# Performance work log

Measured on AMD Instinct MI355X. Metric: run time of the kernel, lower is better.

## Reference

```python
import jax, jax.numpy as jnp
from jax import lax
import numpy as np

N_STEPS = 5  # hard-coded truncated history length in the module


def setup_inputs() -> dict:
    key = jax.random.key(0)
    kH, kv, k1, k2, k3 = jax.random.split(key, 5)
    B, S, D = 32, 512, 512
    scale = 1.0 / np.sqrt(D)  # keep tanh/softmax out of saturation
    return {
        "H": jax.random.normal(kH, (B, S, D), dtype=jnp.float32),
        "v": jax.random.normal(kv, (D, 1), dtype=jnp.float32) * scale,
        "W1": jax.random.normal(k1, (D, D), dtype=jnp.float32) * scale,
        "W2": jax.random.normal(k2, (D, D), dtype=jnp.float32) * scale,
        "W3": jax.random.normal(k3, (D, D), dtype=jnp.float32) * scale,
    }


def reference(H, v, W1, W2, W3):
    # H: [B, S, D] -> output [B, S, D] (torch returns list of S tensors [B,1,D])
    B, S, D = H.shape

    def step(carry, ht):  # ht: [B, D]
        H_prev, H_prev_tilde = carry  # each [B, N_STEPS, D]
        # temp: [B, N_STEPS, D]; ht @ W2 broadcasts over the history axis
        temp = jnp.tanh(H_prev @ W1 + (ht @ W2)[:, None, :] + H_prev_tilde @ W3)
        w_t = jax.nn.softmax(temp @ v, axis=1)            # [B, N_STEPS, 1]
        ht_hat = jnp.sum(H_prev_tilde * w_t, axis=1)      # [B, D]
        ht_tilde = ht + jax.nn.relu(ht_hat)               # [B, D]
        H_prev = jnp.concatenate([H_prev[:, 1:, :], ht[:, None, :]], axis=1)
        H_prev_tilde = jnp.concatenate([H_prev_tilde[:, 1:, :], ht_tilde[:, None, :]], axis=1)
        return (H_prev, H_prev_tilde), ht_tilde

    init = (jnp.zeros((B, N_STEPS, D), H.dtype), jnp.zeros((B, N_STEPS, D), H.dtype))
    _, ys = lax.scan(step, init, jnp.swapaxes(H, 0, 1))  # ys: [S, B, D]
    return jnp.swapaxes(ys, 0, 1)  # [B, S, D]
```

## Files before the change

kernel.cpp:

```cpp
#include <hip/hip_runtime.h>


#define BB 32
#define SS 512
#define DD 512
#define NS 5

#define A_ELEMS    ((size_t)BB * SS * DD)
#define EXCH_U64_PER_B 128
#define EXCH_OFF   (A_ELEMS * 4)
#define EXCH_BYTES ((size_t)BB * EXCH_U64_PER_B * 8)
#define WS_NEED    (EXCH_OFF + EXCH_BYTES)

typedef __attribute__((ext_vector_type(4))) float f32x4;

template <int CTRL, int RMASK, int BMASK, bool BC>
__device__ __forceinline__ float dpp_term(float x) {
  return __uint_as_float((unsigned)__builtin_amdgcn_update_dpp(
      0, (int)__float_as_uint(x), CTRL, RMASK, BMASK, BC));
}
__device__ __forceinline__ float wave_sum64(float x) {
  x += dpp_term<0xB1, 0xF, 0xF, true>(x);
  x += dpp_term<0x4E, 0xF, 0xF, true>(x);
  x += dpp_term<0x141, 0xF, 0xF, true>(x);
  x += dpp_term<0x140, 0xF, 0xF, true>(x);
  x += dpp_term<0x142, 0xA, 0xF, false>(x);
  x += dpp_term<0x143, 0xC, 0xF, false>(x);
  return x;
}
__device__ __forceinline__ float group8_sum(float x) {
  x += dpp_term<0xB1, 0xF, 0xF, true>(x);
  x += dpp_term<0x4E, 0xF, 0xF, true>(x);
  x += dpp_term<0x141, 0xF, 0xF, true>(x);
  return x;
}

__global__ void __launch_bounds__(256) th_phase1(
    const float* __restrict__ H, const float* __restrict__ W1,
    const float* __restrict__ W2, float* __restrict__ A, float* __restrict__ B2) {
  const int tid = threadIdx.x;
  const int mt = blockIdx.x >> 3;
  const int nt = blockIdx.x & 7;
  const int m0 = mt << 6, n0 = nt << 6;
  __shared__ float Ht[64][20];
  __shared__ float Wt1[16][64];
  __shared__ float Wt2[16][64];
  const int tx = tid & 15, ty = tid >> 4;
  const int sr = tid >> 2, sk = (tid & 3) << 2;
  const int wr = tid >> 4, wn = (tid & 15) << 2;
  float a1[4][4] = {{0.f}}, a2[4][4] = {{0.f}};

  for (int k0 = 0; k0 < DD; k0 += 16) {
    float4 hv  = *(const float4*)&H[(size_t)(m0 + sr) * DD + k0 + sk];
    float4 w1v = *(const float4*)&W1[(size_t)(k0 + wr) * DD + n0 + wn];
    float4 w2v = *(const float4*)&W2[(size_t)(k0 + wr) * DD + n0 + wn];
    *(float4*)&Ht[sr][sk]  = hv;
    *(float4*)&Wt1[wr][wn] = w1v;
    *(float4*)&Wt2[wr][wn] = w2v;
    __syncthreads();
#pragma unroll
    for (int kq = 0; kq < 16; kq += 4) {
      float hs[4][4];
#pragma unroll
      for (int i = 0; i < 4; ++i) {
        float4 h4 = *(const float4*)&Ht[ty * 4 + i][kq];
        hs[i][0] = h4.x; hs[i][1] = h4.y; hs[i][2] = h4.z; hs[i][3] = h4.w;
      }
#pragma unroll
      for (int kk = 0; kk < 4; ++kk) {
        float4 w1f = *(const float4*)&Wt1[kq + kk][tx * 4];
        float4 w2f = *(const float4*)&Wt2[kq + kk][tx * 4];
#pragma unroll
        for (int i = 0; i < 4; ++i) {
          float h = hs[i][kk];
          a1[i][0] = fmaf(h, w1f.x, a1[i][0]);
          a1[i][1] = fmaf(h, w1f.y, a1[i][1]);
          a1[i][2] = fmaf(h, w1f.z, a1[i][2]);
          a1[i][3] = fmaf(h, w1f.w, a1[i][3]);
          a2[i][0] = fmaf(h, w2f.x, a2[i][0]);
          a2[i][1] = fmaf(h, w2f.y, a2[i][1]);
          a2[i][2] = fmaf(h, w2f.z, a2[i][2]);
          a2[i][3] = fmaf(h, w2f.w, a2[i][3]);
        }
      }
    }
    __syncthreads();
  }
#pragma unroll
  for (int i = 0; i < 4; ++i) {
    float4 o1 = make_float4(a1[i][0], a1[i][1], a1[i][2], a1[i][3]);
    float4 o2 = make_float4(a2[i][0], a2[i][1], a2[i][2], a2[i][3]);
    size_t off = (size_t)(m0 + ty * 4 + i) * DD + n0 + tx * 4;
    *(float4*)&A[off]  = o1;
    *(float4*)&B2[off] = o2;
  }
}

__global__ void __launch_bounds__(512) th_phase2(
    const float* __restrict__ H, const float* __restrict__ v,
    const float* __restrict__ W3, const float* __restrict__ A,
    float* __restrict__ Ob,
    unsigned long long* __restrict__ exch) {
  const int tid = threadIdx.x;
  const int b = blockIdx.x & 31;
  const int g = blockIdx.x >> 5;
  const int q = tid >> 6;
  const int ln = tid & 63;
  const int col = (g << 6) + ln;

  __shared__ float tlds[DD];
  __shared__ float pm[DD];
  __shared__ float wl[8];

  float wa[64];
#pragma unroll
  for (int i = 0; i < 64; ++i)
    wa[i] = W3[(size_t)(q * 64 + i) * DD + col];

  const float* Hb = H + (size_t)b * SS * DD;
  const float* Ab = A + (size_t)b * SS * DD;
  float* Op = Ob + (size_t)b * SS * DD;
  unsigned long long* eb = exch + (size_t)b * EXCH_U64_PER_B;

  float v_col = (q < NS) ? v[col] : 0.f;
  float aA[NS] = {0.f, 0.f, 0.f, 0.f, 0.f};
  float cC[NS] = {0.f, 0.f, 0.f, 0.f, 0.f};
  float tl[NS] = {0.f, 0.f, 0.f, 0.f, 0.f};
  float s4_prev = 0.f;
  float h_cur = Hb[tid];
  float btB = (q < NS) ? Op[DD + col] : 0.f;

  if (tid < NS) wl[tid] = 0.2f;

#pragma unroll 1
  for (int t5 = 0; t5 < 515; t5 += 5) {
#pragma unroll
    for (int p = 0; p < NS; ++p) {
      const int t = t5 + p;
      if (t < SS) {
        const bool pub = (t + 1 < SS);

        float aN_v = 0.f, bt2 = 0.f;
        if (q < NS) {
          aN_v = Ab[(size_t)t * DD + col];
          if (t + 2 < SS) bt2 = Op[(size_t)(t + 2) * DD + col];
        }
        float h_nxt = 0.f;
        if (pub) h_nxt = Hb[(size_t)(t + 1) * DD + tid];

        if (q >= 1 && q < NS && pub) {
          float aa = aA[(p + 1) % NS];
          aa = (q == 2) ? aA[(p + 2) % NS] : aa;
          aa = (q == 3) ? aA[(p + 3) % NS] : aa;
          aa = (q == 4) ? aA[(p + 4) % NS] : aa;
          float cc = cC[(p + 1) % NS];
          cc = (q == 2) ? cC[(p + 2) % NS] : cc;
          cc = (q == 3) ? cC[(p + 3) % NS] : cc;
          cc = (q == 4) ? cC[(p + 4) % NS] : cc;
          float x = aa + btB + cc;
          float e = __expf(2.0f * x);
          float s = (1.0f - 2.0f / (e + 1.0f)) * v_col;
          s = wave_sum64(s);
          if (ln == 63)
            __hip_atomic_store(&eb[(size_t)((t + 1) & 1) * 64 + (q - 1) * 8 + g],
                (unsigned long long)__float_as_uint(s) |
                    ((unsigned long long)(t + 2) << 32),
                __ATOMIC_RELAXED, __HIP_MEMORY_SCOPE_AGENT);
        }

        if (q == 0 && t >= 1) {
          const unsigned long long* wsl = eb + (size_t)(t & 1) * 64;
          float pv = 0.f;
          if (ln < 40) {
            if (!((ln >> 3) == 4 && (ln & 7) == g)) {
              unsigned long long w;
              do {
                w = __hip_atomic_load(&wsl[ln], __ATOMIC_RELAXED,
                                      __HIP_MEMORY_SCOPE_AGENT);
              } while ((unsigned)(w >> 32) != (unsigned)(t + 1));
              pv = __uint_as_float((unsigned)w);
            } else {
              pv = s4_prev;
            }
          }
          pv = group8_sum(pv);
          float sc0 = __shfl(pv, 0, 64);
          float sc1 = __shfl(pv, 8, 64);
          float sc2 = __shfl(pv, 16, 64);
          float sc3 = __shfl(pv, 24, 64);
          float sc4 = __shfl(pv, 32, 64);
          float mx = fmaxf(fmaxf(fmaxf(sc0, sc1), fmaxf(sc2, sc3)), sc4);
          float e0 = __expf(sc0 - mx), e1 = __expf(sc1 - mx);
          float e2 = __expf(sc2 - mx), e3 = __expf(sc3 - mx);
          float e4 = __expf(sc4 - mx);
          float inv = 1.0f / (e0 + e1 + e2 + e3 + e4);
          float wv = e0 * inv;
          wv = (ln == 1) ? e1 * inv : wv;
          wv = (ln == 2) ? e2 * inv : wv;
          wv = (ln == 3) ? e3 * inv : wv;
          wv = (ln == 4) ? e4 * inv : wv;
          if (ln < NS) wl[ln] = wv;
        }
        __syncthreads();

        float w0 = wl[0], w1 = wl[1], w2 = wl[2], w3_ = wl[3], w4 = wl[4];
        float hh = w0 * tl[p];
        hh = fmaf(w1, tl[(p + 1) % NS], hh);
        hh = fmaf(w2, tl[(p + 2) % NS], hh);
        hh = fmaf(w3_, tl[(p + 3) % NS], hh);
        hh = fmaf(w4, tl[(p + 4) % NS], hh);
        float tld = h_cur + fmaxf(hh, 0.f);
        tl[p] = tld;
        tlds[tid] = tld;
        if (g == 0) Op[(size_t)t * DD + tid] = tld;
        asm volatile("s_waitcnt lgkmcnt(0)" ::: "memory");

        float a0 = 0.f, a1 = 0.f, a2 = 0.f, a3 = 0.f;
        const f32x4* tv = (const f32x4*)&tlds[q << 6];
#pragma unroll
        for (int i = 0; i < 16; ++i) {
          f32x4 t4 = tv[i];
          a0 = fmaf(t4.x, wa[4 * i + 0], a0);
          a1 = fmaf(t4.y, wa[4 * i + 1], a1);
          a2 = fmaf(t4.z, wa[4 * i + 2], a2);
          a3 = fmaf(t4.w, wa[4 * i + 3], a3);
        }
        pm[tid] = (a0 + a1) + (a2 + a3);
        __syncthreads();

        if (q < NS) {
          float c = 0.f;
#pragma unroll
          for (int s = 0; s < 8; ++s) c += pm[s * 64 + ln];
          aA[p] = aN_v;
          cC[p] = c;
          if (q == 0 && pub) {
            float x = aN_v + btB + c;
            float e = __expf(2.0f * x);
            float s4 = (1.0f - 2.0f / (e + 1.0f)) * v_col;
            s4 = wave_sum64(s4);
            if (ln == 63)
              __hip_atomic_store(&eb[(size_t)((t + 1) & 1) * 64 + 32 + g],
                  (unsigned long long)__float_as_uint(s4) |
                      ((unsigned long long)(t + 2) << 32),
                  __ATOMIC_RELAXED, __HIP_MEMORY_SCOPE_AGENT);
            s4_prev = __shfl(s4, 63, 64);
          }
          btB = bt2;
        }
        h_cur = h_nxt;
      }
    }
  }
}

extern "C" void kernel_launch(void* const* d_in, const int* in_sizes, int n_in,
                              void* d_out, int out_size, void* d_ws, size_t ws_size,
                              hipStream_t stream) {
  const float* H  = (const float*)d_in[0];
  const float* v  = (const float*)d_in[1];
  const float* W1 = (const float*)d_in[2];
  const float* W2 = (const float*)d_in[3];
  const float* W3 = (const float*)d_in[4];
  float* out = (float*)d_out;

  if (ws_size < WS_NEED) return;

  float* A = (float*)d_ws;
  unsigned long long* exch = (unsigned long long*)((char*)d_ws + EXCH_OFF);

  (void)hipMemsetAsync(exch, 0, EXCH_BYTES, stream);
  hipLaunchKernelGGL(th_phase1, dim3(256 * 8), dim3(256), 0, stream,
                     H, W1, W2, A, out);
  hipLaunchKernelGGL(th_phase2, dim3(BB * 8), dim3(512), 0, stream,
                     H, v, W3, A, out, exch);
}
```

Before: 1.121 ms.

## Fuse H@W1 and H@W2 projections into the recurrent scan kernel

Removes the separate GEMM pre-pass that computed H@W1 and H@W2 into workspace and output memory. The scan kernel now keeps W1 and W2 column slices in registers alongside W3 and computes the per-step projections inside its loop, using extra shared buffers and a one-step lookahead for the W2 term. This drops a large global write and read of intermediates and one kernel launch. In exchange the sequential critical path per step gains two more 512-wide dot products, and register pressure roughly triples (192 weight floats per thread), which risks spilling.

```diff
diff --git a/kernel.cpp b/kernel.cpp
--- a/kernel.cpp
+++ b/kernel.cpp
@@ -6,11 +6,9 @@
 #define DD 512
 #define NS 5
 
-#define A_ELEMS    ((size_t)BB * SS * DD)
 #define EXCH_U64_PER_B 128
-#define EXCH_OFF   (A_ELEMS * 4)
 #define EXCH_BYTES ((size_t)BB * EXCH_U64_PER_B * 8)
-#define WS_NEED    (EXCH_OFF + EXCH_BYTES)
+#define WS_NEED    EXCH_BYTES
 
 typedef __attribute__((ext_vector_type(4))) float f32x4;
 
@@ -35,70 +33,10 @@
   return x;
 }
 
-__global__ void __launch_bounds__(256) th_phase1(
-    const float* __restrict__ H, const float* __restrict__ W1,
-    const float* __restrict__ W2, float* __restrict__ A, float* __restrict__ B2) {
-  const int tid = threadIdx.x;
-  const int mt = blockIdx.x >> 3;
-  const int nt = blockIdx.x & 7;
-  const int m0 = mt << 6, n0 = nt << 6;
-  __shared__ float Ht[64][20];
-  __shared__ float Wt1[16][64];
-  __shared__ float Wt2[16][64];
-  const int tx = tid & 15, ty = tid >> 4;
-  const int sr = tid >> 2, sk = (tid & 3) << 2;
-  const int wr = tid >> 4, wn = (tid & 15) << 2;
-  float a1[4][4] = {{0.f}}, a2[4][4] = {{0.f}};
-
-  for (int k0 = 0; k0 < DD; k0 += 16) {
-    float4 hv  = *(const float4*)&H[(size_t)(m0 + sr) * DD + k0 + sk];
-    float4 w1v = *(const float4*)&W1[(size_t)(k0 + wr) * DD + n0 + wn];
-    float4 w2v = *(const float4*)&W2[(size_t)(k0 + wr) * DD + n0 + wn];
-    *(float4*)&Ht[sr][sk]  = hv;
-    *(float4*)&Wt1[wr][wn] = w1v;
-    *(float4*)&Wt2[wr][wn] = w2v;
-    __syncthreads();
-#pragma unroll
-    for (int kq = 0; kq < 16; kq += 4) {
-      float hs[4][4];
-#pragma unroll
-      for (int i = 0; i < 4; ++i) {
-        float4 h4 = *(const float4*)&Ht[ty * 4 + i][kq];
-        hs[i][0] = h4.x; hs[i][1] = h4.y; hs[i][2] = h4.z; hs[i][3] = h4.w;
-      }
-#pragma unroll
-      for (int kk = 0; kk < 4; ++kk) {
-        float4 w1f = *(const float4*)&Wt1[kq + kk][tx * 4];
-        float4 w2f = *(const float4*)&Wt2[kq + kk][tx * 4];
-#pragma unroll
-        for (int i = 0; i < 4; ++i) {
-          float h = hs[i][kk];
-          a1[i][0] = fmaf(h, w1f.x, a1[i][0]);
-          a1[i][1] = fmaf(h, w1f.y, a1[i][1]);
-          a1[i][2] = fmaf(h, w1f.z, a1[i][2]);
-          a1[i][3] = fmaf(h, w1f.w, a1[i][3]);
-          a2[i][0] = fmaf(h, w2f.x, a2[i][0]);
-          a2[i][1] = fmaf(h, w2f.y, a2[i][1]);
-          a2[i][2] = fmaf(h, w2f.z, a2[i][2]);
-          a2[i][3] = fmaf(h, w2f.w, a2[i][3]);
-        }
-      }
-    }
-    __syncthreads();
-  }
-#pragma unroll
-  for (int i = 0; i < 4; ++i) {
-    float4 o1 = make_float4(a1[i][0], a1[i][1], a1[i][2], a1[i][3]);
-    float4 o2 = make_float4(a2[i][0], a2[i][1], a2[i][2], a2[i][3]);
-    size_t off = (size_t)(m0 + ty * 4 + i) * DD + n0 + tx * 4;
-    *(float4*)&A[off]  = o1;
-    *(float4*)&B2[off] = o2;
-  }
-}
-
-__global__ void __launch_bounds__(512) th_phase2(
+__global__ void __launch_bounds__(512) th_fused(
     const float* __restrict__ H, const float* __restrict__ v,
-    const float* __restrict__ W3, const float* __restrict__ A,
+    const float* __restrict__ W1, const float* __restrict__ W2,
+    const float* __restrict__ W3,
     float* __restrict__ Ob,
     unsigned long long* __restrict__ exch) {
   const int tid = threadIdx.x;
@@ -109,16 +47,23 @@
   const int col = (g << 6) + ln;
 
   __shared__ float tlds[DD];
-  __shared__ float pm[DD];
+  __shared__ float hA[DD];
+  __shared__ float hB[DD];
+  __shared__ float pm0[DD];
+  __shared__ float pm1[DD];
+  __shared__ float pm2[DD];
   __shared__ float wl[8];
 
-  float wa[64];
-#pragma unroll
-  for (int i = 0; i < 64; ++i)
-    wa[i] = W3[(size_t)(q * 64 + i) * DD + col];
+  float wa3[64], wa1[64], wa2[64];
+#pragma unroll
+  for (int i = 0; i < 64; ++i) {
+    const size_t off = (size_t)(q * 64 + i) * DD + col;
+    wa3[i] = W3[off];
+    wa1[i] = W1[off];
+    wa2[i] = W2[off];
+  }
 
   const float* Hb = H + (size_t)b * SS * DD;
-  const float* Ab = A + (size_t)b * SS * DD;
   float* Op = Ob + (size_t)b * SS * DD;
   unsigned long long* eb = exch + (size_t)b * EXCH_U64_PER_B;
 
@@ -128,9 +73,34 @@
   float tl[NS] = {0.f, 0.f, 0.f, 0.f, 0.f};
   float s4_prev = 0.f;
   float h_cur = Hb[tid];
-  float btB = (q < NS) ? Op[DD + col] : 0.f;
+  float h_n1  = Hb[DD + tid];
+  float btB = 0.f;
 
   if (tid < NS) wl[tid] = 0.2f;
+
+  {
+    hB[tid] = h_n1;
+    asm volatile("s_waitcnt lgkmcnt(0)" ::: "memory");
+    float a0 = 0.f, a1 = 0.f, a2 = 0.f, a3 = 0.f;
+    const f32x4* tv = (const f32x4*)&hB[q << 6];
+#pragma unroll
+    for (int i = 0; i < 16; ++i) {
+      f32x4 t4 = tv[i];
+      a0 = fmaf(t4.x, wa2[4 * i + 0], a0);
+      a1 = fmaf(t4.y, wa2[4 * i + 1], a1);
+      a2 = fmaf(t4.z, wa2[4 * i + 2], a2);
+      a3 = fmaf(t4.w, wa2[4 * i + 3], a3);
+    }
+    pm2[tid] = (a0 + a1) + (a2 + a3);
+    __syncthreads();
+    if (q < NS) {
+      float bb = 0.f;
+#pragma unroll
+      for (int s = 0; s < 8; ++s) bb += pm2[s * 64 + ln];
+      btB = bb;
+    }
+    __syncthreads();
+  }
 
 #pragma unroll 1
   for (int t5 = 0; t5 < 515; t5 += 5) {
@@ -140,13 +110,8 @@
       if (t < SS) {
         const bool pub = (t + 1 < SS);
 
-        float aN_v = 0.f, bt2 = 0.f;
-        if (q < NS) {
-          aN_v = Ab[(size_t)t * DD + col];
-          if (t + 2 < SS) bt2 = Op[(size_t)(t + 2) * DD + col];
-        }
-        float h_nxt = 0.f;
-        if (pub) h_nxt = Hb[(size_t)(t + 1) * DD + tid];
+        float h_n2 = 0.f;
+        if (t + 2 < SS) h_n2 = Hb[(size_t)(t + 2) * DD + tid];
 
         if (q >= 1 && q < NS && pub) {
           float aa = aA[(p + 1) % NS];
@@ -212,30 +177,52 @@
         float tld = h_cur + fmaxf(hh, 0.f);
         tl[p] = tld;
         tlds[tid] = tld;
+        hA[tid] = h_cur;
+        hB[tid] = h_n2;
         if (g == 0) Op[(size_t)t * DD + tid] = tld;
         asm volatile("s_waitcnt lgkmcnt(0)" ::: "memory");
 
-        float a0 = 0.f, a1 = 0.f, a2 = 0.f, a3 = 0.f;
-        const f32x4* tv = (const f32x4*)&tlds[q << 6];
+        float c0 = 0.f, c1 = 0.f, c2 = 0.f, c3 = 0.f;
+        float d0 = 0.f, d1 = 0.f, d2 = 0.f, d3 = 0.f;
+        float f0 = 0.f, f1 = 0.f, f2 = 0.f, f3 = 0.f;
+        const f32x4* tvT = (const f32x4*)&tlds[q << 6];
+        const f32x4* tvA = (const f32x4*)&hA[q << 6];
+        const f32x4* tvB = (const f32x4*)&hB[q << 6];
 #pragma unroll
         for (int i = 0; i < 16; ++i) {
-          f32x4 t4 = tv[i];
-          a0 = fmaf(t4.x, wa[4 * i + 0], a0);
-          a1 = fmaf(t4.y, wa[4 * i + 1], a1);
-          a2 = fmaf(t4.z, wa[4 * i + 2], a2);
-          a3 = fmaf(t4.w, wa[4 * i + 3], a3);
-        }
-        pm[tid] = (a0 + a1) + (a2 + a3);
+          f32x4 tt = tvT[i];
+          f32x4 ta = tvA[i];
+          f32x4 tb = tvB[i];
+          c0 = fmaf(tt.x, wa3[4 * i + 0], c0);
+          c1 = fmaf(tt.y, wa3[4 * i + 1], c1);
+          c2 = fmaf(tt.z, wa3[4 * i + 2], c2);
+          c3 = fmaf(tt.w, wa3[4 * i + 3], c3);
+          d0 = fmaf(ta.x, wa1[4 * i + 0], d0);
+          d1 = fmaf(ta.y, wa1[4 * i + 1], d1);
+          d2 = fmaf(ta.z, wa1[4 * i + 2], d2);
+          d3 = fmaf(ta.w, wa1[4 * i + 3], d3);
+          f0 = fmaf(tb.x, wa2[4 * i + 0], f0);
+          f1 = fmaf(tb.y, wa2[4 * i + 1], f1);
+          f2 = fmaf(tb.z, wa2[4 * i + 2], f2);
+          f3 = fmaf(tb.w, wa2[4 * i + 3], f3);
+        }
+        pm0[tid] = (c0 + c1) + (c2 + c3);
+        pm1[tid] = (d0 + d1) + (d2 + d3);
+        pm2[tid] = (f0 + f1) + (f2 + f3);
         __syncthreads();
 
         if (q < NS) {
-          float c = 0.f;
-#pragma unroll
-          for (int s = 0; s < 8; ++s) c += pm[s * 64 + ln];
-          aA[p] = aN_v;
+          float c = 0.f, a = 0.f, bb = 0.f;
+#pragma unroll
+          for (int s = 0; s < 8; ++s) {
+            c  += pm0[s * 64 + ln];
+            a  += pm1[s * 64 + ln];
+            bb += pm2[s * 64 + ln];
+          }
+          aA[p] = a;
           cC[p] = c;
           if (q == 0 && pub) {
-            float x = aN_v + btB + c;
+            float x = a + btB + c;
             float e = __expf(2.0f * x);
             float s4 = (1.0f - 2.0f / (e + 1.0f)) * v_col;
             s4 = wave_sum64(s4);
@@ -246,9 +233,10 @@
                   __ATOMIC_RELAXED, __HIP_MEMORY_SCOPE_AGENT);
             s4_prev = __shfl(s4, 63, 64);
           }
-          btB = bt2;
-        }
-        h_cur = h_nxt;
+          btB = bb;
+        }
+        h_cur = h_n1;
+        h_n1 = h_n2;
       }
     }
   }
@@ -266,12 +254,9 @@
 
   if (ws_size < WS_NEED) return;
 
-  float* A = (float*)d_ws;
-  unsigned long long* exch = (unsigned long long*)((char*)d_ws + EXCH_OFF);
+  unsigned long long* exch = (unsigned long long*)d_ws;
 
   (void)hipMemsetAsync(exch, 0, EXCH_BYTES, stream);
-  hipLaunchKernelGGL(th_phase1, dim3(256 * 8), dim3(256), 0, stream,
-                     H, W1, W2, A, out);
-  hipLaunchKernelGGL(th_phase2, dim3(BB * 8), dim3(512), 0, stream,
-                     H, v, W3, A, out, exch);
-}
+  hipLaunchKernelGGL(th_fused, dim3(BB * 8), dim3(512), 0, stream,
+                     H, v, W1, W2, W3, out, exch);
+}
```

Result: slower. 2.307 ms (+105.8%).

## Compute ht@W2 inside recurrent kernel using AGPR-resident W2 slice

Applied to the files above, without the earlier changes.

Removes the W2 projection from the phase-1 GEMM, so phase 1 no longer writes it out and phase 2 no longer reads it back. Instead, phase 2 keeps its slice of W2 in accumulation registers and computes the H(t+2)@W2 projection each step, reusing the same LDS broadcast and reduction that the W3 product already uses. This cuts phase-1 work and global traffic but adds matrix-vector FMAs and LDS reads to the serial recurrent loop. It also raises register pressure in that loop.

```diff
diff --git a/kernel.cpp b/kernel.cpp
--- a/kernel.cpp
+++ b/kernel.cpp
@@ -35,28 +35,30 @@
   return x;
 }
 
+#define AGPR_W(dst, src) \
+  asm volatile("v_accvgpr_write_b32 %0, %1" : "=a"(dst) : "v"(src))
+#define AGPR_R(dst, src) \
+  asm volatile("v_accvgpr_read_b32 %0, %1" : "=v"(dst) : "a"(src))
+
 __global__ void __launch_bounds__(256) th_phase1(
     const float* __restrict__ H, const float* __restrict__ W1,
-    const float* __restrict__ W2, float* __restrict__ A, float* __restrict__ B2) {
+    float* __restrict__ A) {
   const int tid = threadIdx.x;
   const int mt = blockIdx.x >> 3;
   const int nt = blockIdx.x & 7;
   const int m0 = mt << 6, n0 = nt << 6;
   __shared__ float Ht[64][20];
   __shared__ float Wt1[16][64];
-  __shared__ float Wt2[16][64];
   const int tx = tid & 15, ty = tid >> 4;
   const int sr = tid >> 2, sk = (tid & 3) << 2;
   const int wr = tid >> 4, wn = (tid & 15) << 2;
-  float a1[4][4] = {{0.f}}, a2[4][4] = {{0.f}};
+  float a1[4][4] = {{0.f}};
 
   for (int k0 = 0; k0 < DD; k0 += 16) {
     float4 hv  = *(const float4*)&H[(size_t)(m0 + sr) * DD + k0 + sk];
     float4 w1v = *(const float4*)&W1[(size_t)(k0 + wr) * DD + n0 + wn];
-    float4 w2v = *(const float4*)&W2[(size_t)(k0 + wr) * DD + n0 + wn];
     *(float4*)&Ht[sr][sk]  = hv;
     *(float4*)&Wt1[wr][wn] = w1v;
-    *(float4*)&Wt2[wr][wn] = w2v;
     __syncthreads();
 #pragma unroll
     for (int kq = 0; kq < 16; kq += 4) {
@@ -69,7 +71,6 @@
 #pragma unroll
       for (int kk = 0; kk < 4; ++kk) {
         float4 w1f = *(const float4*)&Wt1[kq + kk][tx * 4];
-        float4 w2f = *(const float4*)&Wt2[kq + kk][tx * 4];
 #pragma unroll
         for (int i = 0; i < 4; ++i) {
           float h = hs[i][kk];
@@ -77,10 +78,6 @@
           a1[i][1] = fmaf(h, w1f.y, a1[i][1]);
           a1[i][2] = fmaf(h, w1f.z, a1[i][2]);
           a1[i][3] = fmaf(h, w1f.w, a1[i][3]);
-          a2[i][0] = fmaf(h, w2f.x, a2[i][0]);
-          a2[i][1] = fmaf(h, w2f.y, a2[i][1]);
-          a2[i][2] = fmaf(h, w2f.z, a2[i][2]);
-          a2[i][3] = fmaf(h, w2f.w, a2[i][3]);
         }
       }
     }
@@ -89,16 +86,15 @@
 #pragma unroll
   for (int i = 0; i < 4; ++i) {
     float4 o1 = make_float4(a1[i][0], a1[i][1], a1[i][2], a1[i][3]);
-    float4 o2 = make_float4(a2[i][0], a2[i][1], a2[i][2], a2[i][3]);
     size_t off = (size_t)(m0 + ty * 4 + i) * DD + n0 + tx * 4;
-    *(float4*)&A[off]  = o1;
-    *(float4*)&B2[off] = o2;
+    *(float4*)&A[off] = o1;
   }
 }
 
 __global__ void __launch_bounds__(512) th_phase2(
     const float* __restrict__ H, const float* __restrict__ v,
-    const float* __restrict__ W3, const float* __restrict__ A,
+    const float* __restrict__ W2, const float* __restrict__ W3,
+    const float* __restrict__ A,
     float* __restrict__ Ob,
     unsigned long long* __restrict__ exch) {
   const int tid = threadIdx.x;
@@ -109,13 +105,20 @@
   const int col = (g << 6) + ln;
 
   __shared__ float tlds[DD];
+  __shared__ float hB[DD];
   __shared__ float pm[DD];
+  __shared__ float pm2[DD];
   __shared__ float wl[8];
 
   float wa[64];
-#pragma unroll
-  for (int i = 0; i < 64; ++i)
-    wa[i] = W3[(size_t)(q * 64 + i) * DD + col];
+  float ag2[64];
+#pragma unroll
+  for (int i = 0; i < 64; ++i) {
+    const size_t off = (size_t)(q * 64 + i) * DD + col;
+    wa[i] = W3[off];
+    float t2 = W2[off];
+    AGPR_W(ag2[i], t2);
+  }
 
   const float* Hb = H + (size_t)b * SS * DD;
   const float* Ab = A + (size_t)b * SS * DD;
@@ -128,9 +131,39 @@
   float tl[NS] = {0.f, 0.f, 0.f, 0.f, 0.f};
   float s4_prev = 0.f;
   float h_cur = Hb[tid];
-  float btB = (q < NS) ? Op[DD + col] : 0.f;
+  float h_n1  = Hb[DD + tid];
+  float btB = 0.f;
 
   if (tid < NS) wl[tid] = 0.2f;
+
+  {
+    hB[tid] = h_n1;
+    asm volatile("s_waitcnt lgkmcnt(0)" ::: "memory");
+    float a0 = 0.f, a1 = 0.f, a2 = 0.f, a3 = 0.f;
+    const f32x4* tv = (const f32x4*)&hB[q << 6];
+#pragma unroll
+    for (int i = 0; i < 16; ++i) {
+      f32x4 t4 = tv[i];
+      float y0, y1, y2, y3;
+      AGPR_R(y0, ag2[4 * i + 0]);
+      AGPR_R(y1, ag2[4 * i + 1]);
+      AGPR_R(y2, ag2[4 * i + 2]);
+      AGPR_R(y3, ag2[4 * i + 3]);
+      a0 = fmaf(t4.x, y0, a0);
+      a1 = fmaf(t4.y, y1, a1);
+      a2 = fmaf(t4.z, y2, a2);
+      a3 = fmaf(t4.w, y3, a3);
+    }
+    pm2[tid] = (a0 + a1) + (a2 + a3);
+    __syncthreads();
+    if (q < NS) {
+      float bb = 0.f;
+#pragma unroll
+      for (int s = 0; s < 8; ++s) bb += pm2[s * 64 + ln];
+      btB = bb;
+    }
+    __syncthreads();
+  }
 
 #pragma unroll 1
   for (int t5 = 0; t5 < 515; t5 += 5) {
@@ -140,13 +173,10 @@
       if (t < SS) {
         const bool pub = (t + 1 < SS);
 
-        float aN_v = 0.f, bt2 = 0.f;
-        if (q < NS) {
-          aN_v = Ab[(size_t)t * DD + col];
-          if (t + 2 < SS) bt2 = Op[(size_t)(t + 2) * DD + col];
-        }
-        float h_nxt = 0.f;
-        if (pub) h_nxt = Hb[(size_t)(t + 1) * DD + tid];
+        float aN_v = 0.f;
+        if (q < NS) aN_v = Ab[(size_t)t * DD + col];
+        float h_n2 = 0.f;
+        if (t + 2 < SS) h_n2 = Hb[(size_t)(t + 2) * DD + tid];
 
         if (q >= 1 && q < NS && pub) {
           float aa = aA[(p + 1) % NS];
@@ -212,26 +242,43 @@
         float tld = h_cur + fmaxf(hh, 0.f);
         tl[p] = tld;
         tlds[tid] = tld;
+        hB[tid] = h_n2;
         if (g == 0) Op[(size_t)t * DD + tid] = tld;
         asm volatile("s_waitcnt lgkmcnt(0)" ::: "memory");
 
         float a0 = 0.f, a1 = 0.f, a2 = 0.f, a3 = 0.f;
-        const f32x4* tv = (const f32x4*)&tlds[q << 6];
+        float f0 = 0.f, f1 = 0.f, f2 = 0.f, f3 = 0.f;
+        const f32x4* tvT = (const f32x4*)&tlds[q << 6];
+        const f32x4* tvB = (const f32x4*)&hB[q << 6];
 #pragma unroll
         for (int i = 0; i < 16; ++i) {
-          f32x4 t4 = tv[i];
-          a0 = fmaf(t4.x, wa[4 * i + 0], a0);
-          a1 = fmaf(t4.y, wa[4 * i + 1], a1);
-          a2 = fmaf(t4.z, wa[4 * i + 2], a2);
-          a3 = fmaf(t4.w, wa[4 * i + 3], a3);
-        }
-        pm[tid] = (a0 + a1) + (a2 + a3);
+          f32x4 tt = tvT[i];
+          f32x4 tb = tvB[i];
+          a0 = fmaf(tt.x, wa[4 * i + 0], a0);
+          a1 = fmaf(tt.y, wa[4 * i + 1], a1);
+          a2 = fmaf(tt.z, wa[4 * i + 2], a2);
+          a3 = fmaf(tt.w, wa[4 * i + 3], a3);
+          float y0, y1, y2, y3;
+          AGPR_R(y0, ag2[4 * i + 0]);
+          AGPR_R(y1, ag2[4 * i + 1]);
+          AGPR_R(y2, ag2[4 * i + 2]);
+          AGPR_R(y3, ag2[4 * i + 3]);
+          f0 = fmaf(tb.x, y0, f0);
+          f1 = fmaf(tb.y, y1, f1);
+          f2 = fmaf(tb.z, y2, f2);
+          f3 = fmaf(tb.w, y3, f3);
+        }
+        pm[tid]  = (a0 + a1) + (a2 + a3);
+        pm2[tid] = (f0 + f1) + (f2 + f3);
         __syncthreads();
 
         if (q < NS) {
-          float c = 0.f;
-#pragma unroll
-          for (int s = 0; s < 8; ++s) c += pm[s * 64 + ln];
+          float c = 0.f, bb = 0.f;
+#pragma unroll
+          for (int s = 0; s < 8; ++s) {
+            c  += pm[s * 64 + ln];
+            bb += pm2[s * 64 + ln];
+          }
           aA[p] = aN_v;
           cC[p] = c;
           if (q == 0 && pub) {
@@ -246,9 +293,10 @@
                   __ATOMIC_RELAXED, __HIP_MEMORY_SCOPE_AGENT);
             s4_prev = __shfl(s4, 63, 64);
           }
-          btB = bt2;
-        }
-        h_cur = h_nxt;
+          btB = bb;
+        }
+        h_cur = h_n1;
+        h_n1 = h_n2;
       }
     }
   }
@@ -271,7 +319,7 @@
 
   (void)hipMemsetAsync(exch, 0, EXCH_BYTES, stream);
   hipLaunchKernelGGL(th_phase1, dim3(256 * 8), dim3(256), 0, stream,
-                     H, W1, W2, A, out);
+                     H, W1, A);
   hipLaunchKernelGGL(th_phase2, dim3(BB * 8), dim3(512), 0, stream,
-                     H, v, W3, A, out, exch);
-}
+                     H, v, W2, W3, A, out, exch);
+}
```

New measurement: 2.879 ms. 157% more time.

## Fuse input projections into recurrent kernel using bf16 MFMA

Applied to the files above, without the earlier changes.

Removes the separate fp32 SIMT GEMM kernel that computed H@W1 and H@W2. The recurrent kernel now computes these projections at its start, using bf16 16x16x32 MFMA instructions. Each block computes only the batch/column slice it later consumes, so no cross-block dependency is added. The output row for t=0 is written one step late, so the precomputed W2 term stored there is not overwritten before it is read. This trades fp32 accuracy for bf16 inputs and uses uncached, strided global loads of W without LDS staging.

```diff
diff --git a/kernel.cpp b/kernel.cpp
--- a/kernel.cpp
+++ b/kernel.cpp
@@ -13,6 +13,7 @@
 #define WS_NEED    (EXCH_OFF + EXCH_BYTES)
 
 typedef __attribute__((ext_vector_type(4))) float f32x4;
+typedef __attribute__((ext_vector_type(8))) __bf16 bf16x8;
 
 template <int CTRL, int RMASK, int BMASK, bool BC>
 __device__ __forceinline__ float dpp_term(float x) {
@@ -35,70 +36,11 @@
   return x;
 }
 
-__global__ void __launch_bounds__(256) th_phase1(
-    const float* __restrict__ H, const float* __restrict__ W1,
-    const float* __restrict__ W2, float* __restrict__ A, float* __restrict__ B2) {
-  const int tid = threadIdx.x;
-  const int mt = blockIdx.x >> 3;
-  const int nt = blockIdx.x & 7;
-  const int m0 = mt << 6, n0 = nt << 6;
-  __shared__ float Ht[64][20];
-  __shared__ float Wt1[16][64];
-  __shared__ float Wt2[16][64];
-  const int tx = tid & 15, ty = tid >> 4;
-  const int sr = tid >> 2, sk = (tid & 3) << 2;
-  const int wr = tid >> 4, wn = (tid & 15) << 2;
-  float a1[4][4] = {{0.f}}, a2[4][4] = {{0.f}};
-
-  for (int k0 = 0; k0 < DD; k0 += 16) {
-    float4 hv  = *(const float4*)&H[(size_t)(m0 + sr) * DD + k0 + sk];
-    float4 w1v = *(const float4*)&W1[(size_t)(k0 + wr) * DD + n0 + wn];
-    float4 w2v = *(const float4*)&W2[(size_t)(k0 + wr) * DD + n0 + wn];
-    *(float4*)&Ht[sr][sk]  = hv;
-    *(float4*)&Wt1[wr][wn] = w1v;
-    *(float4*)&Wt2[wr][wn] = w2v;
-    __syncthreads();
-#pragma unroll
-    for (int kq = 0; kq < 16; kq += 4) {
-      float hs[4][4];
-#pragma unroll
-      for (int i = 0; i < 4; ++i) {
-        float4 h4 = *(const float4*)&Ht[ty * 4 + i][kq];
-        hs[i][0] = h4.x; hs[i][1] = h4.y; hs[i][2] = h4.z; hs[i][3] = h4.w;
-      }
-#pragma unroll
-      for (int kk = 0; kk < 4; ++kk) {
-        float4 w1f = *(const float4*)&Wt1[kq + kk][tx * 4];
-        float4 w2f = *(const float4*)&Wt2[kq + kk][tx * 4];
-#pragma unroll
-        for (int i = 0; i < 4; ++i) {
-          float h = hs[i][kk];
-          a1[i][0] = fmaf(h, w1f.x, a1[i][0]);
-          a1[i][1] = fmaf(h, w1f.y, a1[i][1]);
-          a1[i][2] = fmaf(h, w1f.z, a1[i][2]);
-          a1[i][3] = fmaf(h, w1f.w, a1[i][3]);
-          a2[i][0] = fmaf(h, w2f.x, a2[i][0]);
-          a2[i][1] = fmaf(h, w2f.y, a2[i][1]);
-          a2[i][2] = fmaf(h, w2f.z, a2[i][2]);
-          a2[i][3] = fmaf(h, w2f.w, a2[i][3]);
-        }
-      }
-    }
-    __syncthreads();
-  }
-#pragma unroll
-  for (int i = 0; i < 4; ++i) {
-    float4 o1 = make_float4(a1[i][0], a1[i][1], a1[i][2], a1[i][3]);
-    float4 o2 = make_float4(a2[i][0], a2[i][1], a2[i][2], a2[i][3]);
-    size_t off = (size_t)(m0 + ty * 4 + i) * DD + n0 + tx * 4;
-    *(float4*)&A[off]  = o1;
-    *(float4*)&B2[off] = o2;
-  }
-}
-
 __global__ void __launch_bounds__(512) th_phase2(
     const float* __restrict__ H, const float* __restrict__ v,
-    const float* __restrict__ W3, const float* __restrict__ A,
+    const float* __restrict__ W1, const float* __restrict__ W2,
+    const float* __restrict__ W3,
+    float* __restrict__ A,
     float* __restrict__ Ob,
     unsigned long long* __restrict__ exch) {
   const int tid = threadIdx.x;
@@ -112,21 +54,76 @@
   __shared__ float pm[DD];
   __shared__ float wl[8];
 
+  const float* Hb = H + (size_t)b * SS * DD;
+  float* Ab = A + (size_t)b * SS * DD;
+  float* Op = Ob + (size_t)b * SS * DD;
+  unsigned long long* eb = exch + (size_t)b * EXCH_U64_PER_B;
+
+  {
+    const int lm = ln & 15;
+    const int lkb = (ln >> 4) << 3;
+    const int lr4 = (ln >> 4) << 2;
+#pragma unroll 1
+    for (int mat = 0; mat < 2; ++mat) {
+      const float* Wm = mat ? W2 : W1;
+      float* Out = mat ? Op : Ab;
+      f32x4 acc[4][4];
+#pragma unroll
+      for (int x = 0; x < 4; ++x)
+#pragma unroll
+        for (int y = 0; y < 4; ++y)
+          acc[x][y] = (f32x4){0.f, 0.f, 0.f, 0.f};
+#pragma unroll 1
+      for (int s = 0; s < 16; ++s) {
+        const int kb = s * 32 + lkb;
+        bf16x8 af[4];
+#pragma unroll
+        for (int mt = 0; mt < 4; ++mt) {
+          const float* hp = Hb + (size_t)(q * 64 + mt * 16 + lm) * DD + kb;
+          float4 u0 = *(const float4*)hp;
+          float4 u1 = *(const float4*)(hp + 4);
+          bf16x8 t;
+          t[0] = (__bf16)u0.x; t[1] = (__bf16)u0.y;
+          t[2] = (__bf16)u0.z; t[3] = (__bf16)u0.w;
+          t[4] = (__bf16)u1.x; t[5] = (__bf16)u1.y;
+          t[6] = (__bf16)u1.z; t[7] = (__bf16)u1.w;
+          af[mt] = t;
+        }
+#pragma unroll
+        for (int nt = 0; nt < 4; ++nt) {
+          const float* wp = Wm + (size_t)kb * DD + (g * 64 + nt * 16 + lm);
+          bf16x8 bfr;
+#pragma unroll
+          for (int i = 0; i < 8; ++i) bfr[i] = (__bf16)wp[(size_t)i * DD];
+#pragma unroll
+          for (int mt = 0; mt < 4; ++mt)
+            acc[mt][nt] = __builtin_amdgcn_mfma_f32_16x16x32_bf16(
+                af[mt], bfr, acc[mt][nt], 0, 0, 0);
+        }
+      }
+#pragma unroll
+      for (int mt = 0; mt < 4; ++mt)
+#pragma unroll
+        for (int nt = 0; nt < 4; ++nt)
+#pragma unroll
+          for (int i = 0; i < 4; ++i)
+            Out[(size_t)(q * 64 + mt * 16 + lr4 + i) * DD +
+                (g * 64 + nt * 16 + lm)] = acc[mt][nt][i];
+    }
+    __syncthreads();
+  }
+
   float wa[64];
 #pragma unroll
   for (int i = 0; i < 64; ++i)
     wa[i] = W3[(size_t)(q * 64 + i) * DD + col];
-
-  const float* Hb = H + (size_t)b * SS * DD;
-  const float* Ab = A + (size_t)b * SS * DD;
-  float* Op = Ob + (size_t)b * SS * DD;
-  unsigned long long* eb = exch + (size_t)b * EXCH_U64_PER_B;
 
   float v_col = (q < NS) ? v[col] : 0.f;
   float aA[NS] = {0.f, 0.f, 0.f, 0.f, 0.f};
   float cC[NS] = {0.f, 0.f, 0.f, 0.f, 0.f};
   float tl[NS] = {0.f, 0.f, 0.f, 0.f, 0.f};
   float s4_prev = 0.f;
+  float tld0 = 0.f;
   float h_cur = Hb[tid];
   float btB = (q < NS) ? Op[DD + col] : 0.f;
 
@@ -212,7 +209,14 @@
         float tld = h_cur + fmaxf(hh, 0.f);
         tl[p] = tld;
         tlds[tid] = tld;
-        if (g == 0) Op[(size_t)t * DD + tid] = tld;
+        if (g == 0) {
+          if (t == 0) {
+            tld0 = tld;
+          } else {
+            Op[(size_t)t * DD + tid] = tld;
+            if (t == 1) Op[tid] = tld0;
+          }
+        }
         asm volatile("s_waitcnt lgkmcnt(0)" ::: "memory");
 
         float a0 = 0.f, a1 = 0.f, a2 = 0.f, a3 = 0.f;
@@ -270,8 +274,6 @@
   unsigned long long* exch = (unsigned long long*)((char*)d_ws + EXCH_OFF);
 
   (void)hipMemsetAsync(exch, 0, EXCH_BYTES, stream);
-  hipLaunchKernelGGL(th_phase1, dim3(256 * 8), dim3(256), 0, stream,
-                     H, W1, W2, A, out);
   hipLaunchKernelGGL(th_phase2, dim3(BB * 8), dim3(512), 0, stream,
-                     H, v, W3, A, out, exch);
-}
+                     H, v, W1, W2, W3, A, out, exch);
+}
```

New measurement: 977.7 us. 1.15x faster.
